# Optimization experiments

Measured on AMD Instinct MI355X. Metric: run time of the kernel, lower is better.

The kernel has to match this reference:

```python
import jax, jax.numpy as jnp
import numpy as np

# Hyperparameters (from init_kwargs)
N = 100000      # num_nodes
T = 4           # num_edge_type
E = 400000      # edges per type
C = 2           # num_channels
L = 2           # num_layers
W_IN = 128      # input feature dim
D = 64          # node_dim (w_out)
NUM_CLASS = 16
BETA = 0.5
M = 10000       # number of target nodes


def setup_inputs() -> dict:
    key = jax.random.key(0)
    ks = jax.random.split(key, 10)
    glorot = np.sqrt(6.0 / (W_IN + D))
    glorot1 = np.sqrt(6.0 / (C * D + D))
    glorot2 = np.sqrt(6.0 / (D + NUM_CLASS))
    return {
        "X": jax.random.normal(ks[0], (N, W_IN), dtype=jnp.float32),
        "edge_value": jax.random.uniform(ks[1], (T, E), dtype=jnp.float32),
        "conv_weights": 0.1 * jax.random.normal(ks[2], (L, C, T), dtype=jnp.float32),
        "Ws": jax.random.uniform(ks[3], (C, W_IN, D), minval=-glorot, maxval=glorot, dtype=jnp.float32),
        "lin1_w": jax.random.uniform(ks[4], (C * D, D), minval=-glorot1, maxval=glorot1, dtype=jnp.float32),
        "lin1_b": jnp.zeros((D,), dtype=jnp.float32),
        "lin_w": jax.random.uniform(ks[5], (D, NUM_CLASS), minval=-glorot2, maxval=glorot2, dtype=jnp.float32),
        "lin_b": jnp.zeros((NUM_CLASS,), dtype=jnp.float32),
        "edge_index": jax.random.randint(ks[6], (T, 2, E), 0, N),
        "target_x": jax.random.randint(ks[7], (M,), 0, N),
    }


def reference(X, edge_value, conv_weights, Ws, lin1_w, lin1_b, lin_w, lin_b,
              edge_index, target_x):
    # Flatten edge types into one big edge list. torch_sparse.coalesce(op='add')
    # followed by torch.sparse.mm is mathematically a duplicate-summing SpMM,
    # i.e. a segment_sum over destination rows.
    rows = edge_index[:, 0, :].reshape(-1)      # [T*E]
    cols = edge_index[:, 1, :].reshape(-1)      # [T*E]
    vals = edge_value.reshape(-1)               # [T*E]
    type_id = jnp.repeat(jnp.arange(T), E)      # [T*E] edge-type id (constant)

    # Per-channel input projections: X_ = X @ Ws[c]  -> [C, N, D]
    X_ = jnp.einsum('nf,cfd->cnd', X, Ws)
    H = X_

    for l in range(L):
        # FastGTConv: softmax over edge types per channel
        filt = jax.nn.softmax(conv_weights[l], axis=1)   # [C, T]
        newH = []
        for c in range(C):
            v = vals * filt[c, type_id]                  # [T*E] mixed edge weights
            msgs = v[:, None] * H[c][cols]               # gather + scale: [T*E, D]
            newH.append(jax.ops.segment_sum(msgs, rows, num_segments=N))
        H = jnp.stack(newH)                              # [C, N, D]

    # FastGTN tail: relu(beta*X_ + (1-beta)*H), concat channels, linear1
    Hc = jax.nn.relu(BETA * X_ + (1.0 - BETA) * H)       # [C, N, D]
    Hcat = jnp.transpose(Hc, (1, 0, 2)).reshape(N, C * D)
    H_ = Hcat @ lin1_w + lin1_b                          # [N, D]

    # FastGTNs head: logits at target nodes
    return H_[target_x] @ lin_w + lin_b                  # [M, NUM_CLASS]
```

## Files before the change

kernel.cpp:

```cpp
#include <hip/hip_runtime.h>

#define N_NODES   100000
#define T_TYPES   4
#define E_EDGES   400000
#define E4        100000
#define G_TOT     400000
#define TE_TOT    1600000
#define C_CH      2
#define L_LAYERS  2
#define W_INF     128
#define DD        64
#define NUM_CLASS 16
#define BETA      0.5f
#define M_TGT     10000

#define NBKT      391
#define BROWS     256
#define BPAD      4864
#define CHUNK_G   1024
#define NPART_BLK 391
#define PROJ_BLK  1563

static const size_t PLANE2 = (size_t)N_NODES * DD;

typedef __attribute__((ext_vector_type(8))) short short8x;
typedef __attribute__((ext_vector_type(4))) float f32x4;

__device__ __forceinline__ unsigned bf16rne(float x) {
    unsigned u = __float_as_uint(x);
    return (u + 0x7FFFu + ((u >> 16) & 1u)) >> 16;
}
__device__ __forceinline__ unsigned packbf(float a, float b) {
    return bf16rne(a) | (bf16rne(b) << 16);
}
__device__ __forceinline__ float bflo(unsigned u) { return __uint_as_float(u << 16); }
__device__ __forceinline__ float bfhi(unsigned u) { return __uint_as_float(u & 0xFFFF0000u); }

__device__ __forceinline__ void load_filter(const float* cw, int layer,
                                            float* f0, float* f1) {
    float m0 = -1e30f, m1 = -1e30f;
    #pragma unroll
    for (int t = 0; t < T_TYPES; ++t) {
        f0[t] = cw[layer * C_CH * T_TYPES + t];
        f1[t] = cw[layer * C_CH * T_TYPES + T_TYPES + t];
        m0 = fmaxf(m0, f0[t]); m1 = fmaxf(m1, f1[t]);
    }
    float s0 = 0.f, s1 = 0.f;
    #pragma unroll
    for (int t = 0; t < T_TYPES; ++t) {
        f0[t] = __expf(f0[t] - m0); s0 += f0[t];
        f1[t] = __expf(f1[t] - m1); s1 += f1[t];
    }
    #pragma unroll
    for (int t = 0; t < T_TYPES; ++t) { f0[t] /= s0; f1[t] /= s1; }
}

__global__ void prep_kernel(const float* __restrict__ Ws,
                            unsigned short* __restrict__ Wsb,
                            int* __restrict__ cursor) {
    int b = blockIdx.x;
    int tid = threadIdx.x;
    if (b < 64) {
        int idx = b * 256 + tid;
        int c   = idx >> 13;
        int rem = idx & 8191;
        int d   = rem >> 7;
        int k   = rem & 127;
        Wsb[idx] = (unsigned short)bf16rne(Ws[c * (W_INF * DD) + k * DD + d]);
    } else {
        int idx = (b - 64) * 256 + tid;
        if (idx < NBKT) cursor[idx] = idx * BPAD;
    }
}

#define AROW 136
#define SMEM_BYTES 45664

__global__ __launch_bounds__(256) void build_proj_kernel(
        const int* __restrict__ edge_index,
        const float* __restrict__ edge_value,
        const float* __restrict__ cw,
        int* __restrict__ cursor,
        int2* __restrict__ edata2,
        const float* __restrict__ X,
        const unsigned short* __restrict__ Wsb,
        unsigned* __restrict__ Xp16) {
    __shared__ __align__(16) char smem[SMEM_BYTES];
    int tid = threadIdx.x;

    if (blockIdx.x < NPART_BLK) {
        int* cnt   = (int*)smem;
        int* lbase = cnt + 392;
        int* gbase = lbase + 392;
        int2* le   = (int2*)(smem + 4704);
        unsigned short* lbk = (unsigned short*)(smem + 4704 + 32768);

        int p = blockIdx.x;
        for (int j = tid; j < NBKT; j += 256) cnt[j] = 0;
        __syncthreads();

        float f0[T_TYPES], f1[T_TYPES];
        load_filter(cw, 0, f0, f1);

        int px[16], pv[16], rk[16], bk[16];
        int ne = 0;
        #pragma unroll
        for (int g = 0; g < 4; ++g) {
            int idx = p * CHUNK_G + g * 256 + tid;
            if (idx < G_TOT) {
                int t = idx / E4, r = idx - t * E4;
                const int* bptr = edge_index + (size_t)t * 2 * E_EDGES;
                int4   rw = ((const int4*)bptr)[r];
                int4   cl = ((const int4*)(bptr + E_EDGES))[r];
                float4 vv = ((const float4*)(edge_value + (size_t)t * E_EDGES))[r];
                int tb = t << 17;
                int   rr[4] = {rw.x, rw.y, rw.z, rw.w};
                int   cc[4] = {cl.x, cl.y, cl.z, cl.w};
                float vf[4] = {vv.x, vv.y, vv.z, vv.w};
                #pragma unroll
                for (int k = 0; k < 4; ++k) {
                    int b = rr[k] >> 8;
                    px[ne] = cc[k] | tb | ((rr[k] & 255) << 19);
                    pv[ne] = __float_as_int(vf[k]);
                    bk[ne] = b;
                    rk[ne] = atomicAdd(&cnt[b], 1);
                    ++ne;
                }
            }
        }
        __syncthreads();
        if (tid < 64) {
            int c[7]; int s = 0;
            #pragma unroll
            for (int k = 0; k < 7; ++k) {
                int idx = tid * 7 + k;
                c[k] = (idx < NBKT) ? cnt[idx] : 0;
                s += c[k];
            }
            int inc = s;
            #pragma unroll
            for (int off = 1; off < 64; off <<= 1) {
                int v = __shfl_up(inc, off);
                if (tid >= off) inc += v;
            }
            int base = inc - s;
            #pragma unroll
            for (int k = 0; k < 7; ++k) {
                int idx = tid * 7 + k;
                if (idx < NBKT) lbase[idx] = base;
                base += c[k];
            }
        }
        __syncthreads();
        #pragma unroll
        for (int k = 0; k < 16; ++k) {
            if (k < ne) {
                int slot = lbase[bk[k]] + rk[k];
                le[slot]  = make_int2(px[k], pv[k]);
                lbk[slot] = (unsigned short)bk[k];
            }
        }
        __syncthreads();
        for (int j = tid; j < NBKT; j += 256)
            gbase[j] = cnt[j] ? atomicAdd(&cursor[j], cnt[j]) : 0;
        __syncthreads();
        int ngrp = min(CHUNK_G, G_TOT - p * CHUNK_G);
        int nloc = 4 * ngrp;
        for (int j = tid; j < nloc; j += 256) {
            int b = lbk[j];
            int2 e = le[j];
            int t = (e.x >> 17) & 3;
            float v = __int_as_float(e.y);
            edata2[gbase[b] + (j - lbase[b])] =
                make_int2(e.x, (int)packbf(v * f0[t], v * f1[t]));
        }
    } else {
        unsigned short* a_lds = (unsigned short*)smem;
        int row0 = (blockIdx.x - NPART_BLK) * 64;

        const float4* X4 = (const float4*)X;
        #pragma unroll
        for (int i = 0; i < 8; ++i) {
            int gi = tid + 256 * i;
            int r  = gi >> 5;
            int c4 = gi & 31;
            int row = row0 + r;
            float4 v = make_float4(0.f, 0.f, 0.f, 0.f);
            if (row < N_NODES) v = X4[(size_t)row * 32 + c4];
            *(uint2*)&a_lds[r * AROW + c4 * 4] = make_uint2(packbf(v.x, v.y),
                                                            packbf(v.z, v.w));
        }
        __syncthreads();

        int wave = tid >> 6, lane = tid & 63;
        int m = lane & 15, q = lane >> 4;

        short8x A[4];
        #pragma unroll
        for (int ks = 0; ks < 4; ++ks)
            A[ks] = *(const short8x*)&a_lds[(wave * 16 + m) * AROW + ks * 32 + q * 8];

        #pragma unroll
        for (int ct = 0; ct < 4; ++ct) {
            f32x4 acc0 = {0.f, 0.f, 0.f, 0.f};
            f32x4 acc1 = {0.f, 0.f, 0.f, 0.f};
            #pragma unroll
            for (int ks = 0; ks < 4; ++ks) {
                short8x B0 = *(const short8x*)(Wsb + (ct * 16 + m) * 128 + ks * 32 + q * 8);
                short8x B1 = *(const short8x*)(Wsb + 8192 + (ct * 16 + m) * 128 + ks * 32 + q * 8);
                acc0 = __builtin_amdgcn_mfma_f32_16x16x32_bf16(A[ks], B0, acc0, 0, 0, 0);
                acc1 = __builtin_amdgcn_mfma_f32_16x16x32_bf16(A[ks], B1, acc1, 0, 0, 0);
            }
            #pragma unroll
            for (int r = 0; r < 4; ++r) {
                int row = row0 + wave * 16 + q * 4 + r;
                if (row < N_NODES)
                    Xp16[(size_t)row * DD + ct * 16 + m] = packbf(acc0[r], acc1[r]);
            }
        }
    }
}

__global__ __launch_bounds__(512) void rowsort_kernel(const int* __restrict__ cursor,
                                                      int2* __restrict__ edata2,
                                                      int* __restrict__ offs) {
    __shared__ int rcnt[BROWS];
    __shared__ int rbase[BROWS];
    __shared__ int rcur[BROWS];
    __shared__ int2 le[BPAD];
    int b   = blockIdx.x;
    int tid = threadIdx.x;
    int bb  = b * BPAD;
    int cnt = cursor[b] - bb;
    if (tid < BROWS) rcnt[tid] = 0;
    __syncthreads();
    for (int j = tid; j < cnt; j += 512) {
        int2 e = edata2[bb + j];
        le[j] = e;
        atomicAdd(&rcnt[(e.x >> 19) & 255], 1);
    }
    __syncthreads();
    if (tid < 64) {
        int c[4]; int s = 0;
        #pragma unroll
        for (int k = 0; k < 4; ++k) { c[k] = rcnt[tid * 4 + k]; s += c[k]; }
        int inc = s;
        #pragma unroll
        for (int off = 1; off < 64; off <<= 1) {
            int v = __shfl_up(inc, off);
            if (tid >= off) inc += v;
        }
        int base = inc - s;
        #pragma unroll
        for (int k = 0; k < 4; ++k) { rbase[tid * 4 + k] = base; base += c[k]; }
    }
    __syncthreads();
    if (tid < BROWS) rcur[tid] = rbase[tid];
    __syncthreads();
    for (int j = tid; j < cnt; j += 512) {
        int2 e = le[j];
        int lr = (e.x >> 19) & 255;
        int pos = atomicAdd(&rcur[lr], 1);
        edata2[bb + pos] = e;
    }
    int row0  = b * BROWS;
    int nrows = min(BROWS, N_NODES - row0);
    if (tid < nrows)
        offs[row0 + tid] = bb + rbase[tid] + rcnt[tid];
}

__device__ __forceinline__ void qfma(const uint4 h, unsigned wp,
                                     float4& a, float4& b) {
    float w0 = bflo(wp), w1 = bfhi(wp);
    a.x = fmaf(w0, bflo(h.x), a.x);
    a.y = fmaf(w1, bfhi(h.x), a.y);
    a.z = fmaf(w0, bflo(h.y), a.z);
    a.w = fmaf(w1, bfhi(h.y), a.w);
    b.x = fmaf(w0, bflo(h.z), b.x);
    b.y = fmaf(w1, bfhi(h.z), b.y);
    b.z = fmaf(w0, bflo(h.w), b.z);
    b.w = fmaf(w1, bfhi(h.w), b.w);
}

__device__ __forceinline__ void qreduce(float4& a, float4& b) {
    a.x += __shfl_xor(a.x, 16); a.y += __shfl_xor(a.y, 16);
    a.z += __shfl_xor(a.z, 16); a.w += __shfl_xor(a.w, 16);
    b.x += __shfl_xor(b.x, 16); b.y += __shfl_xor(b.y, 16);
    b.z += __shfl_xor(b.z, 16); b.w += __shfl_xor(b.w, 16);
    a.x += __shfl_xor(a.x, 32); a.y += __shfl_xor(a.y, 32);
    a.z += __shfl_xor(a.z, 32); a.w += __shfl_xor(a.w, 32);
    b.x += __shfl_xor(b.x, 32); b.y += __shfl_xor(b.y, 32);
    b.z += __shfl_xor(b.z, 32); b.w += __shfl_xor(b.w, 32);
}

__device__ __forceinline__ int row_beg(const int* offs, int row) {
    return ((row & 255) == 0) ? (row >> 8) * BPAD : offs[row - 1];
}

__global__ __launch_bounds__(256) void spmm_gather(const unsigned* __restrict__ Hin16,
                                                   unsigned* __restrict__ Hout16,
                                                   const int* __restrict__ offs,
                                                   const int2* __restrict__ edata2) {
    int lane = threadIdx.x & 63;
    int s16 = lane & 15, sub = lane >> 4;
    int row  = (blockIdx.x * blockDim.x + threadIdx.x) >> 6;
    int beg = row_beg(offs, row);
    int end = offs[row];
    const uint4* hp = (const uint4*)Hin16;
    float4 a = make_float4(0.f, 0.f, 0.f, 0.f);
    float4 b = make_float4(0.f, 0.f, 0.f, 0.f);
    int i = beg + sub;
    for (; i + 4 < end; i += 8) {
        int2 e0 = edata2[i];
        int2 e1 = edata2[i + 4];
        uint4 h0 = hp[(size_t)(e0.x & 0x1FFFF) * 16 + s16];
        uint4 h1 = hp[(size_t)(e1.x & 0x1FFFF) * 16 + s16];
        qfma(h0, (unsigned)e0.y, a, b);
        qfma(h1, (unsigned)e1.y, a, b);
    }
    if (i < end) {
        int2 e = edata2[i];
        uint4 h = hp[(size_t)(e.x & 0x1FFFF) * 16 + s16];
        qfma(h, (unsigned)e.y, a, b);
    }
    qreduce(a, b);
    if (sub == 0)
        ((uint4*)Hout16)[(size_t)row * 16 + s16] =
            make_uint4(packbf(a.x, a.y), packbf(a.z, a.w),
                       packbf(b.x, b.y), packbf(b.z, b.w));
}

__global__ __launch_bounds__(256) void tgt_tail_kernel(const unsigned* __restrict__ Hin16,
                                                       const unsigned* __restrict__ Xp16,
                                                       const int* __restrict__ offs,
                                                       const int2* __restrict__ edata2,
                                                       const float* __restrict__ cw,
                                                       const int* __restrict__ tgt,
                                                       const float* __restrict__ lin1_w,
                                                       const float* __restrict__ lin1_b,
                                                       const float* __restrict__ lin_w,
                                                       const float* __restrict__ lin_b,
                                                       float* __restrict__ out) {
    __shared__ float l1w[W_INF * DD];
    __shared__ float lw[DD * NUM_CLASS];
    __shared__ float l1b[DD];
    __shared__ float lb[NUM_CLASS];
    __shared__ float hc[4][W_INF];
    __shared__ float hmid[4][DD];

    int tid = threadIdx.x;
    {
        const float4* g = (const float4*)lin1_w;
        float4* s = (float4*)l1w;
        #pragma unroll
        for (int i = 0; i < 8; ++i) s[tid + 256 * i] = g[tid + 256 * i];
        ((float4*)lw)[tid] = ((const float4*)lin_w)[tid];
        if (tid < DD) l1b[tid] = lin1_b[tid];
        else if (tid < DD + NUM_CLASS) lb[tid - DD] = lin_b[tid - DD];
    }

    float f0a[T_TYPES], f1a[T_TYPES], f0b[T_TYPES], f1b[T_TYPES];
    load_filter(cw, 0, f0a, f1a);
    load_filter(cw, 1, f0b, f1b);
    float r0[T_TYPES], r1[T_TYPES];
    #pragma unroll
    for (int t = 0; t < T_TYPES; ++t) { r0[t] = f0b[t] / f0a[t]; r1[t] = f1b[t] / f1a[t]; }

    int w = tid >> 6, lane = tid & 63;
    int s16 = lane & 15, sub = lane >> 4;
    int m = blockIdx.x * 4 + w;
    int row = tgt[m];
    int beg = row_beg(offs, row);
    int end = offs[row];
    const uint4* hp = (const uint4*)Hin16;
    float4 a = make_float4(0.f, 0.f, 0.f, 0.f);
    float4 b = make_float4(0.f, 0.f, 0.f, 0.f);
    for (int i = beg + sub; i < end; i += 4) {
        int2 e = edata2[i];
        int t = (e.x >> 17) & 3;
        uint4 h = hp[(size_t)(e.x & 0x1FFFF) * 16 + s16];
        unsigned wp = (unsigned)e.y;
        float w0 = bflo(wp) * r0[t], w1 = bfhi(wp) * r1[t];
        a.x = fmaf(w0, bflo(h.x), a.x);
        a.y = fmaf(w1, bfhi(h.x), a.y);
        a.z = fmaf(w0, bflo(h.y), a.z);
        a.w = fmaf(w1, bfhi(h.y), a.w);
        b.x = fmaf(w0, bflo(h.z), b.x);
        b.y = fmaf(w1, bfhi(h.z), b.y);
        b.z = fmaf(w0, bflo(h.w), b.z);
        b.w = fmaf(w1, bfhi(h.w), b.w);
    }
    qreduce(a, b);

    if (sub == 0) {
        uint4 xu = ((const uint4*)Xp16)[(size_t)row * 16 + s16];
        int d0 = 4 * s16;
        hc[w][d0 + 0]      = fmaxf(BETA * bflo(xu.x) + (1.f - BETA) * a.x, 0.f);
        hc[w][DD + d0 + 0] = fmaxf(BETA * bfhi(xu.x) + (1.f - BETA) * a.y, 0.f);
        hc[w][d0 + 1]      = fmaxf(BETA * bflo(xu.y) + (1.f - BETA) * a.z, 0.f);
        hc[w][DD + d0 + 1] = fmaxf(BETA * bfhi(xu.y) + (1.f - BETA) * a.w, 0.f);
        hc[w][d0 + 2]      = fmaxf(BETA * bflo(xu.z) + (1.f - BETA) * b.x, 0.f);
        hc[w][DD + d0 + 2] = fmaxf(BETA * bfhi(xu.z) + (1.f - BETA) * b.y, 0.f);
        hc[w][d0 + 3]      = fmaxf(BETA * bflo(xu.w) + (1.f - BETA) * b.z, 0.f);
        hc[w][DD + d0 + 3] = fmaxf(BETA * bfhi(xu.w) + (1.f - BETA) * b.w, 0.f);
    }
    __syncthreads();

    float a1 = l1b[lane];
    #pragma unroll 8
    for (int k = 0; k < W_INF; ++k)
        a1 = fmaf(hc[w][k], l1w[k * DD + lane], a1);
    hmid[w][lane] = a1;
    __syncthreads();

    if (lane < NUM_CLASS) {
        float o = lb[lane];
        #pragma unroll 8
        for (int k = 0; k < DD; ++k)
            o = fmaf(hmid[w][k], lw[k * NUM_CLASS + lane], o);
        out[(size_t)m * NUM_CLASS + lane] = o;
    }
}

extern "C" void kernel_launch(void* const* d_in, const int* in_sizes, int n_in,
                              void* d_out, int out_size, void* d_ws, size_t ws_size,
                              hipStream_t stream) {
    const float* X            = (const float*)d_in[0];
    const float* edge_value   = (const float*)d_in[1];
    const float* conv_weights = (const float*)d_in[2];
    const float* Ws           = (const float*)d_in[3];
    const float* lin1_w       = (const float*)d_in[4];
    const float* lin1_b       = (const float*)d_in[5];
    const float* lin_w        = (const float*)d_in[6];
    const float* lin_b        = (const float*)d_in[7];
    const int*   edge_index   = (const int*)d_in[8];
    const int*   target_x     = (const int*)d_in[9];
    float* out = (float*)d_out;

    unsigned*       Xp16 = (unsigned*)d_ws;
    unsigned*       H116 = Xp16 + PLANE2;
    unsigned short* Wsb  = (unsigned short*)(H116 + PLANE2);
    int*            offs = (int*)(Wsb + C_CH * W_INF * DD);
    int*            cursor = offs + N_NODES;
    int2*           edata2 = (int2*)(cursor + 512);

    prep_kernel<<<66, 256, 0, stream>>>(Ws, Wsb, cursor);
    build_proj_kernel<<<NPART_BLK + PROJ_BLK, 256, 0, stream>>>(
        edge_index, edge_value, conv_weights, cursor, edata2, X, Wsb, Xp16);
    rowsort_kernel<<<NBKT, 512, 0, stream>>>(cursor, edata2, offs);
    spmm_gather<<<(N_NODES * 64) / 256, 256, 0, stream>>>(Xp16, H116, offs, edata2);
    tgt_tail_kernel<<<M_TGT / 4, 256, 0, stream>>>(H116, Xp16, offs, edata2,
                                                   conv_weights, target_x,
                                                   lin1_w, lin1_b, lin_w, lin_b, out);
}
```

Measured before the change: 251.9 us.

## Use 64-row buckets and fuse row sort into SpMM gather kernel

```diff
diff --git a/kernel.cpp b/kernel.cpp
--- a/kernel.cpp
+++ b/kernel.cpp
@@ -5,18 +5,16 @@
 #define E_EDGES   400000
 #define E4        100000
 #define G_TOT     400000
-#define TE_TOT    1600000
 #define C_CH      2
-#define L_LAYERS  2
 #define W_INF     128
 #define DD        64
 #define NUM_CLASS 16
 #define BETA      0.5f
 #define M_TGT     10000
 
-#define NBKT      391
-#define BROWS     256
-#define BPAD      4864
+#define NSB       1563
+#define NSB_PAD   1568
+#define SBPAD     1408
 #define CHUNK_G   1024
 #define NPART_BLK 391
 #define PROJ_BLK  1563
@@ -69,12 +67,9 @@
         Wsb[idx] = (unsigned short)bf16rne(Ws[c * (W_INF * DD) + k * DD + d]);
     } else {
         int idx = (b - 64) * 256 + tid;
-        if (idx < NBKT) cursor[idx] = idx * BPAD;
-    }
-}
-
-#define AROW 136
-#define SMEM_BYTES 45664
+        if (idx < NSB) cursor[idx] = idx * SBPAD;
+    }
+}
 
 __global__ __launch_bounds__(256) void build_proj_kernel(
         const int* __restrict__ edge_index,
@@ -85,120 +80,80 @@
         const float* __restrict__ X,
         const unsigned short* __restrict__ Wsb,
         unsigned* __restrict__ Xp16) {
-    __shared__ __align__(16) char smem[SMEM_BYTES];
+    __shared__ int cnt[NSB_PAD];
+    __shared__ int gbase[NSB_PAD];
     int tid = threadIdx.x;
 
     if (blockIdx.x < NPART_BLK) {
-        int* cnt   = (int*)smem;
-        int* lbase = cnt + 392;
-        int* gbase = lbase + 392;
-        int2* le   = (int2*)(smem + 4704);
-        unsigned short* lbk = (unsigned short*)(smem + 4704 + 32768);
-
         int p = blockIdx.x;
-        for (int j = tid; j < NBKT; j += 256) cnt[j] = 0;
+        for (int j = tid; j < NSB; j += 256) cnt[j] = 0;
         __syncthreads();
 
         float f0[T_TYPES], f1[T_TYPES];
         load_filter(cw, 0, f0, f1);
 
-        int px[16], pv[16], rk[16], bk[16];
-        int ne = 0;
+        int px[16], rk[16], bk[16];
+        bool gv[4];
         #pragma unroll
         for (int g = 0; g < 4; ++g) {
             int idx = p * CHUNK_G + g * 256 + tid;
-            if (idx < G_TOT) {
+            gv[g] = idx < G_TOT;
+            if (gv[g]) {
                 int t = idx / E4, r = idx - t * E4;
                 const int* bptr = edge_index + (size_t)t * 2 * E_EDGES;
-                int4   rw = ((const int4*)bptr)[r];
-                int4   cl = ((const int4*)(bptr + E_EDGES))[r];
+                int4 rw = ((const int4*)bptr)[r];
+                int4 cl = ((const int4*)(bptr + E_EDGES))[r];
+                int tb = t << 17;
+                int rr[4] = {rw.x, rw.y, rw.z, rw.w};
+                int cc[4] = {cl.x, cl.y, cl.z, cl.w};
+                #pragma unroll
+                for (int k = 0; k < 4; ++k) {
+                    int kk = g * 4 + k;
+                    int b = rr[k] >> 6;
+                    px[kk] = cc[k] | tb | ((rr[k] & 63) << 19);
+                    bk[kk] = b;
+                    rk[kk] = atomicAdd(&cnt[b], 1);
+                }
+            }
+        }
+        __syncthreads();
+        for (int j = tid; j < NSB; j += 256)
+            gbase[j] = cnt[j] ? atomicAdd(&cursor[j], cnt[j]) : 0;
+        __syncthreads();
+        #pragma unroll
+        for (int g = 0; g < 4; ++g) {
+            if (gv[g]) {
+                int idx = p * CHUNK_G + g * 256 + tid;
+                int t = idx / E4, r = idx - t * E4;
                 float4 vv = ((const float4*)(edge_value + (size_t)t * E_EDGES))[r];
-                int tb = t << 17;
-                int   rr[4] = {rw.x, rw.y, rw.z, rw.w};
-                int   cc[4] = {cl.x, cl.y, cl.z, cl.w};
                 float vf[4] = {vv.x, vv.y, vv.z, vv.w};
                 #pragma unroll
                 for (int k = 0; k < 4; ++k) {
-                    int b = rr[k] >> 8;
-                    px[ne] = cc[k] | tb | ((rr[k] & 255) << 19);
-                    pv[ne] = __float_as_int(vf[k]);
-                    bk[ne] = b;
-                    rk[ne] = atomicAdd(&cnt[b], 1);
-                    ++ne;
+                    int kk = g * 4 + k;
+                    int tt = (px[kk] >> 17) & 3;
+                    edata2[(size_t)gbase[bk[kk]] + rk[kk]] =
+                        make_int2(px[kk], (int)packbf(vf[k] * f0[tt], vf[k] * f1[tt]));
                 }
             }
         }
-        __syncthreads();
-        if (tid < 64) {
-            int c[7]; int s = 0;
-            #pragma unroll
-            for (int k = 0; k < 7; ++k) {
-                int idx = tid * 7 + k;
-                c[k] = (idx < NBKT) ? cnt[idx] : 0;
-                s += c[k];
-            }
-            int inc = s;
-            #pragma unroll
-            for (int off = 1; off < 64; off <<= 1) {
-                int v = __shfl_up(inc, off);
-                if (tid >= off) inc += v;
-            }
-            int base = inc - s;
-            #pragma unroll
-            for (int k = 0; k < 7; ++k) {
-                int idx = tid * 7 + k;
-                if (idx < NBKT) lbase[idx] = base;
-                base += c[k];
-            }
-        }
-        __syncthreads();
-        #pragma unroll
-        for (int k = 0; k < 16; ++k) {
-            if (k < ne) {
-                int slot = lbase[bk[k]] + rk[k];
-                le[slot]  = make_int2(px[k], pv[k]);
-                lbk[slot] = (unsigned short)bk[k];
-            }
-        }
-        __syncthreads();
-        for (int j = tid; j < NBKT; j += 256)
-            gbase[j] = cnt[j] ? atomicAdd(&cursor[j], cnt[j]) : 0;
-        __syncthreads();
-        int ngrp = min(CHUNK_G, G_TOT - p * CHUNK_G);
-        int nloc = 4 * ngrp;
-        for (int j = tid; j < nloc; j += 256) {
-            int b = lbk[j];
-            int2 e = le[j];
-            int t = (e.x >> 17) & 3;
-            float v = __int_as_float(e.y);
-            edata2[gbase[b] + (j - lbase[b])] =
-                make_int2(e.x, (int)packbf(v * f0[t], v * f1[t]));
-        }
     } else {
-        unsigned short* a_lds = (unsigned short*)smem;
         int row0 = (blockIdx.x - NPART_BLK) * 64;
-
-        const float4* X4 = (const float4*)X;
-        #pragma unroll
-        for (int i = 0; i < 8; ++i) {
-            int gi = tid + 256 * i;
-            int r  = gi >> 5;
-            int c4 = gi & 31;
-            int row = row0 + r;
-            float4 v = make_float4(0.f, 0.f, 0.f, 0.f);
-            if (row < N_NODES) v = X4[(size_t)row * 32 + c4];
-            *(uint2*)&a_lds[r * AROW + c4 * 4] = make_uint2(packbf(v.x, v.y),
-                                                            packbf(v.z, v.w));
-        }
-        __syncthreads();
-
         int wave = tid >> 6, lane = tid & 63;
         int m = lane & 15, q = lane >> 4;
-
-        short8x A[4];
-        #pragma unroll
-        for (int ks = 0; ks < 4; ++ks)
-            A[ks] = *(const short8x*)&a_lds[(wave * 16 + m) * AROW + ks * 32 + q * 8];
+        int arow = row0 + wave * 16 + m;
+        const float4* X4 = (const float4*)X;
+        union { short8x s; uint4 u; } A[4];
+        bool valid = arow < N_NODES;
+        #pragma unroll
+        for (int ks = 0; ks < 4; ++ks) {
+            float4 va = make_float4(0.f, 0.f, 0.f, 0.f), vb = va;
+            if (valid) {
+                va = X4[(size_t)arow * 32 + ks * 8 + q * 2];
+                vb = X4[(size_t)arow * 32 + ks * 8 + q * 2 + 1];
+            }
+            A[ks].u = make_uint4(packbf(va.x, va.y), packbf(va.z, va.w),
+                                 packbf(vb.x, vb.y), packbf(vb.z, vb.w));
+        }
 
         #pragma unroll
         for (int ct = 0; ct < 4; ++ct) {
@@ -208,8 +163,8 @@
             for (int ks = 0; ks < 4; ++ks) {
                 short8x B0 = *(const short8x*)(Wsb + (ct * 16 + m) * 128 + ks * 32 + q * 8);
                 short8x B1 = *(const short8x*)(Wsb + 8192 + (ct * 16 + m) * 128 + ks * 32 + q * 8);
-                acc0 = __builtin_amdgcn_mfma_f32_16x16x32_bf16(A[ks], B0, acc0, 0, 0, 0);
-                acc1 = __builtin_amdgcn_mfma_f32_16x16x32_bf16(A[ks], B1, acc1, 0, 0, 0);
+                acc0 = __builtin_amdgcn_mfma_f32_16x16x32_bf16(A[ks].s, B0, acc0, 0, 0, 0);
+                acc1 = __builtin_amdgcn_mfma_f32_16x16x32_bf16(A[ks].s, B1, acc1, 0, 0, 0);
             }
             #pragma unroll
             for (int r = 0; r < 4; ++r) {
@@ -219,54 +174,6 @@
             }
         }
     }
-}
-
-__global__ __launch_bounds__(512) void rowsort_kernel(const int* __restrict__ cursor,
-                                                      int2* __restrict__ edata2,
-                                                      int* __restrict__ offs) {
-    __shared__ int rcnt[BROWS];
-    __shared__ int rbase[BROWS];
-    __shared__ int rcur[BROWS];
-    __shared__ int2 le[BPAD];
-    int b   = blockIdx.x;
-    int tid = threadIdx.x;
-    int bb  = b * BPAD;
-    int cnt = cursor[b] - bb;
-    if (tid < BROWS) rcnt[tid] = 0;
-    __syncthreads();
-    for (int j = tid; j < cnt; j += 512) {
-        int2 e = edata2[bb + j];
-        le[j] = e;
-        atomicAdd(&rcnt[(e.x >> 19) & 255], 1);
-    }
-    __syncthreads();
-    if (tid < 64) {
-        int c[4]; int s = 0;
-        #pragma unroll
-        for (int k = 0; k < 4; ++k) { c[k] = rcnt[tid * 4 + k]; s += c[k]; }
-        int inc = s;
-        #pragma unroll
-        for (int off = 1; off < 64; off <<= 1) {
-            int v = __shfl_up(inc, off);
-            if (tid >= off) inc += v;
-        }
-        int base = inc - s;
-        #pragma unroll
-        for (int k = 0; k < 4; ++k) { rbase[tid * 4 + k] = base; base += c[k]; }
-    }
-    __syncthreads();
-    if (tid < BROWS) rcur[tid] = rbase[tid];
-    __syncthreads();
-    for (int j = tid; j < cnt; j += 512) {
-        int2 e = le[j];
-        int lr = (e.x >> 19) & 255;
-        int pos = atomicAdd(&rcur[lr], 1);
-        edata2[bb + pos] = e;
-    }
-    int row0  = b * BROWS;
-    int nrows = min(BROWS, N_NODES - row0);
-    if (tid < nrows)
-        offs[row0 + tid] = bb + rbase[tid] + rcnt[tid];
 }
 
 __device__ __forceinline__ void qfma(const uint4 h, unsigned wp,
@@ -294,40 +201,86 @@
 }
 
 __device__ __forceinline__ int row_beg(const int* offs, int row) {
-    return ((row & 255) == 0) ? (row >> 8) * BPAD : offs[row - 1];
-}
-
-__global__ __launch_bounds__(256) void spmm_gather(const unsigned* __restrict__ Hin16,
-                                                   unsigned* __restrict__ Hout16,
-                                                   const int* __restrict__ offs,
-                                                   const int2* __restrict__ edata2) {
-    int lane = threadIdx.x & 63;
+    return ((row & 63) == 0) ? (row >> 6) * SBPAD : offs[row - 1];
+}
+
+__global__ __launch_bounds__(256) void sortgather_kernel(
+        const int* __restrict__ cursor,
+        int2* __restrict__ edata2,
+        int* __restrict__ offs,
+        const unsigned* __restrict__ Hin16,
+        unsigned* __restrict__ Hout16) {
+    __shared__ int rcnt[64];
+    __shared__ int rbase[64];
+    __shared__ int rcur[64];
+    __shared__ int2 ls[SBPAD];
+    int tid = threadIdx.x;
+    int sb = blockIdx.x;
+    int base = sb * SBPAD;
+    int cntb = cursor[sb] - base;
+
+    if (tid < 64) rcnt[tid] = 0;
+    __syncthreads();
+    for (int j = tid; j < cntb; j += 256)
+        atomicAdd(&rcnt[(edata2[base + j].x >> 19) & 63], 1);
+    __syncthreads();
+    if (tid < 64) {
+        int c = rcnt[tid];
+        int inc = c;
+        #pragma unroll
+        for (int off = 1; off < 64; off <<= 1) {
+            int v = __shfl_up(inc, off);
+            if (tid >= off) inc += v;
+        }
+        rbase[tid] = inc - c;
+        rcur[tid]  = inc - c;
+    }
+    __syncthreads();
+    for (int j = tid; j < cntb; j += 256) {
+        int2 e = edata2[base + j];
+        int pos = atomicAdd(&rcur[(e.x >> 19) & 63], 1);
+        ls[pos] = e;
+    }
+    __syncthreads();
+
+    for (int j = tid; j < cntb; j += 256) edata2[base + j] = ls[j];
+    int row0 = sb << 6;
+    if (tid < 64) {
+        int row = row0 + tid;
+        if (row < N_NODES) offs[row] = base + rbase[tid] + rcnt[tid];
+    }
+
+    int wv = tid >> 6, lane = tid & 63;
     int s16 = lane & 15, sub = lane >> 4;
-    int row  = (blockIdx.x * blockDim.x + threadIdx.x) >> 6;
-    int beg = row_beg(offs, row);
-    int end = offs[row];
     const uint4* hp = (const uint4*)Hin16;
-    float4 a = make_float4(0.f, 0.f, 0.f, 0.f);
-    float4 b = make_float4(0.f, 0.f, 0.f, 0.f);
-    int i = beg + sub;
-    for (; i + 4 < end; i += 8) {
-        int2 e0 = edata2[i];
-        int2 e1 = edata2[i + 4];
-        uint4 h0 = hp[(size_t)(e0.x & 0x1FFFF) * 16 + s16];
-        uint4 h1 = hp[(size_t)(e1.x & 0x1FFFF) * 16 + s16];
-        qfma(h0, (unsigned)e0.y, a, b);
-        qfma(h1, (unsigned)e1.y, a, b);
-    }
-    if (i < end) {
-        int2 e = edata2[i];
-        uint4 h = hp[(size_t)(e.x & 0x1FFFF) * 16 + s16];
-        qfma(h, (unsigned)e.y, a, b);
-    }
-    qreduce(a, b);
-    if (sub == 0)
-        ((uint4*)Hout16)[(size_t)row * 16 + s16] =
-            make_uint4(packbf(a.x, a.y), packbf(a.z, a.w),
-                       packbf(b.x, b.y), packbf(b.z, b.w));
+    #pragma unroll 1
+    for (int t16 = 0; t16 < 16; ++t16) {
+        int lr = wv * 16 + t16;
+        int beg = rbase[lr];
+        int end = beg + rcnt[lr];
+        float4 a = make_float4(0.f, 0.f, 0.f, 0.f);
+        float4 b = make_float4(0.f, 0.f, 0.f, 0.f);
+        int i = beg + sub;
+        for (; i + 4 < end; i += 8) {
+            int2 e0 = ls[i];
+            int2 e1 = ls[i + 4];
+            uint4 h0 = hp[(size_t)(e0.x & 0x1FFFF) * 16 + s16];
+            uint4 h1 = hp[(size_t)(e1.x & 0x1FFFF) * 16 + s16];
+            qfma(h0, (unsigned)e0.y, a, b);
+            qfma(h1, (unsigned)e1.y, a, b);
+        }
+        if (i < end) {
+            int2 e = ls[i];
+            uint4 h = hp[(size_t)(e.x & 0x1FFFF) * 16 + s16];
+            qfma(h, (unsigned)e.y, a, b);
+        }
+        qreduce(a, b);
+        int row = row0 + lr;
+        if (sub == 0 && row < N_NODES)
+            ((uint4*)Hout16)[(size_t)row * 16 + s16] =
+                make_uint4(packbf(a.x, a.y), packbf(a.z, a.w),
+                           packbf(b.x, b.y), packbf(b.z, b.w));
+    }
 }
 
 __global__ __launch_bounds__(256) void tgt_tail_kernel(const unsigned* __restrict__ Hin16,
@@ -442,13 +395,12 @@
     unsigned short* Wsb  = (unsigned short*)(H116 + PLANE2);
     int*            offs = (int*)(Wsb + C_CH * W_INF * DD);
     int*            cursor = offs + N_NODES;
-    int2*           edata2 = (int2*)(cursor + 512);
-
-    prep_kernel<<<66, 256, 0, stream>>>(Ws, Wsb, cursor);
+    int2*           edata2 = (int2*)(cursor + 1600);
+
+    prep_kernel<<<71, 256, 0, stream>>>(Ws, Wsb, cursor);
     build_proj_kernel<<<NPART_BLK + PROJ_BLK, 256, 0, stream>>>(
         edge_index, edge_value, conv_weights, cursor, edata2, X, Wsb, Xp16);
-    rowsort_kernel<<<NBKT, 512, 0, stream>>>(cursor, edata2, offs);
-    spmm_gather<<<(N_NODES * 64) / 256, 256, 0, stream>>>(Xp16, H116, offs, edata2);
+    sortgather_kernel<<<NSB, 256, 0, stream>>>(cursor, edata2, offs, Xp16, H116);
     tgt_tail_kernel<<<M_TGT / 4, 256, 0, stream>>>(H116, Xp16, offs, edata2,
                                                    conv_weights, target_x,
                                                    lin1_w, lin1_b, lin_w, lin_b, out);
```

Result: no change. 251.9 us (+0.0%).

## Fuse row sort into layer-1 SpMM gather, shrink partition chunks, drop projection LDS staging

Applied to the files above, without the earlier changes.

```diff
diff --git a/kernel.cpp b/kernel.cpp
--- a/kernel.cpp
+++ b/kernel.cpp
@@ -5,9 +5,7 @@
 #define E_EDGES   400000
 #define E4        100000
 #define G_TOT     400000
-#define TE_TOT    1600000
 #define C_CH      2
-#define L_LAYERS  2
 #define W_INF     128
 #define DD        64
 #define NUM_CLASS 16
@@ -17,8 +15,8 @@
 #define NBKT      391
 #define BROWS     256
 #define BPAD      4864
-#define CHUNK_G   1024
-#define NPART_BLK 391
+#define CHUNK_G   512
+#define NPART_BLK 782
 #define PROJ_BLK  1563
 
 static const size_t PLANE2 = (size_t)N_NODES * DD;
@@ -73,9 +71,6 @@
     }
 }
 
-#define AROW 136
-#define SMEM_BYTES 45664
-
 __global__ __launch_bounds__(256) void build_proj_kernel(
         const int* __restrict__ edge_index,
         const float* __restrict__ edge_value,
@@ -85,16 +80,14 @@
         const float* __restrict__ X,
         const unsigned short* __restrict__ Wsb,
         unsigned* __restrict__ Xp16) {
-    __shared__ __align__(16) char smem[SMEM_BYTES];
+    __shared__ int cnt[392];
+    __shared__ int lbase[392];
+    __shared__ int gbase[392];
+    __shared__ int2 le[2048];
+    __shared__ unsigned short lbk[2048];
     int tid = threadIdx.x;
 
     if (blockIdx.x < NPART_BLK) {
-        int* cnt   = (int*)smem;
-        int* lbase = cnt + 392;
-        int* gbase = lbase + 392;
-        int2* le   = (int2*)(smem + 4704);
-        unsigned short* lbk = (unsigned short*)(smem + 4704 + 32768);
-
         int p = blockIdx.x;
         for (int j = tid; j < NBKT; j += 256) cnt[j] = 0;
         __syncthreads();
@@ -102,10 +95,10 @@
         float f0[T_TYPES], f1[T_TYPES];
         load_filter(cw, 0, f0, f1);
 
-        int px[16], pv[16], rk[16], bk[16];
+        int px[8], pv[8], rk[8], bk[8];
         int ne = 0;
         #pragma unroll
-        for (int g = 0; g < 4; ++g) {
+        for (int g = 0; g < 2; ++g) {
             int idx = p * CHUNK_G + g * 256 + tid;
             if (idx < G_TOT) {
                 int t = idx / E4, r = idx - t * E4;
@@ -153,7 +146,7 @@
         }
         __syncthreads();
         #pragma unroll
-        for (int k = 0; k < 16; ++k) {
+        for (int k = 0; k < 8; ++k) {
             if (k < ne) {
                 int slot = lbase[bk[k]] + rk[k];
                 le[slot]  = make_int2(px[k], pv[k]);
@@ -175,30 +168,23 @@
                 make_int2(e.x, (int)packbf(v * f0[t], v * f1[t]));
         }
     } else {
-        unsigned short* a_lds = (unsigned short*)smem;
         int row0 = (blockIdx.x - NPART_BLK) * 64;
-
-        const float4* X4 = (const float4*)X;
-        #pragma unroll
-        for (int i = 0; i < 8; ++i) {
-            int gi = tid + 256 * i;
-            int r  = gi >> 5;
-            int c4 = gi & 31;
-            int row = row0 + r;
-            float4 v = make_float4(0.f, 0.f, 0.f, 0.f);
-            if (row < N_NODES) v = X4[(size_t)row * 32 + c4];
-            *(uint2*)&a_lds[r * AROW + c4 * 4] = make_uint2(packbf(v.x, v.y),
-                                                            packbf(v.z, v.w));
-        }
-        __syncthreads();
-
         int wave = tid >> 6, lane = tid & 63;
         int m = lane & 15, q = lane >> 4;
-
-        short8x A[4];
-        #pragma unroll
-        for (int ks = 0; ks < 4; ++ks)
-            A[ks] = *(const short8x*)&a_lds[(wave * 16 + m) * AROW + ks * 32 + q * 8];
+        int arow = row0 + wave * 16 + m;
+        const float4* X4 = (const float4*)X;
+        union { short8x s; uint4 u; } A[4];
+        bool valid = arow < N_NODES;
+        #pragma unroll
+        for (int ks = 0; ks < 4; ++ks) {
+            float4 va = make_float4(0.f, 0.f, 0.f, 0.f), vb = va;
+            if (valid) {
+                va = X4[(size_t)arow * 32 + ks * 8 + q * 2];
+                vb = X4[(size_t)arow * 32 + ks * 8 + q * 2 + 1];
+            }
+            A[ks].u = make_uint4(packbf(va.x, va.y), packbf(va.z, va.w),
+                                 packbf(vb.x, vb.y), packbf(vb.z, vb.w));
+        }
 
         #pragma unroll
         for (int ct = 0; ct < 4; ++ct) {
@@ -208,8 +194,8 @@
             for (int ks = 0; ks < 4; ++ks) {
                 short8x B0 = *(const short8x*)(Wsb + (ct * 16 + m) * 128 + ks * 32 + q * 8);
                 short8x B1 = *(const short8x*)(Wsb + 8192 + (ct * 16 + m) * 128 + ks * 32 + q * 8);
-                acc0 = __builtin_amdgcn_mfma_f32_16x16x32_bf16(A[ks], B0, acc0, 0, 0, 0);
-                acc1 = __builtin_amdgcn_mfma_f32_16x16x32_bf16(A[ks], B1, acc1, 0, 0, 0);
+                acc0 = __builtin_amdgcn_mfma_f32_16x16x32_bf16(A[ks].s, B0, acc0, 0, 0, 0);
+                acc1 = __builtin_amdgcn_mfma_f32_16x16x32_bf16(A[ks].s, B1, acc1, 0, 0, 0);
             }
             #pragma unroll
             for (int r = 0; r < 4; ++r) {
@@ -219,54 +205,6 @@
             }
         }
     }
-}
-
-__global__ __launch_bounds__(512) void rowsort_kernel(const int* __restrict__ cursor,
-                                                      int2* __restrict__ edata2,
-                                                      int* __restrict__ offs) {
-    __shared__ int rcnt[BROWS];
-    __shared__ int rbase[BROWS];
-    __shared__ int rcur[BROWS];
-    __shared__ int2 le[BPAD];
-    int b   = blockIdx.x;
-    int tid = threadIdx.x;
-    int bb  = b * BPAD;
-    int cnt = cursor[b] - bb;
-    if (tid < BROWS) rcnt[tid] = 0;
-    __syncthreads();
-    for (int j = tid; j < cnt; j += 512) {
-        int2 e = edata2[bb + j];
-        le[j] = e;
-        atomicAdd(&rcnt[(e.x >> 19) & 255], 1);
-    }
-    __syncthreads();
-    if (tid < 64) {
-        int c[4]; int s = 0;
-        #pragma unroll
-        for (int k = 0; k < 4; ++k) { c[k] = rcnt[tid * 4 + k]; s += c[k]; }
-        int inc = s;
-        #pragma unroll
-        for (int off = 1; off < 64; off <<= 1) {
-            int v = __shfl_up(inc, off);
-            if (tid >= off) inc += v;
-        }
-        int base = inc - s;
-        #pragma unroll
-        for (int k = 0; k < 4; ++k) { rbase[tid * 4 + k] = base; base += c[k]; }
-    }
-    __syncthreads();
-    if (tid < BROWS) rcur[tid] = rbase[tid];
-    __syncthreads();
-    for (int j = tid; j < cnt; j += 512) {
-        int2 e = le[j];
-        int lr = (e.x >> 19) & 255;
-        int pos = atomicAdd(&rcur[lr], 1);
-        edata2[bb + pos] = e;
-    }
-    int row0  = b * BROWS;
-    int nrows = min(BROWS, N_NODES - row0);
-    if (tid < nrows)
-        offs[row0 + tid] = bb + rbase[tid] + rcnt[tid];
 }
 
 __device__ __forceinline__ void qfma(const uint4 h, unsigned wp,
@@ -297,40 +235,95 @@
     return ((row & 255) == 0) ? (row >> 8) * BPAD : offs[row - 1];
 }
 
-__global__ __launch_bounds__(256) void spmm_gather(const unsigned* __restrict__ Hin16,
-                                                   unsigned* __restrict__ Hout16,
-                                                   const int* __restrict__ offs,
-                                                   const int2* __restrict__ edata2) {
-    int lane = threadIdx.x & 63;
+__global__ __launch_bounds__(512) void sortgather_kernel(
+        const int* __restrict__ cursor,
+        int2* __restrict__ edata2,
+        int* __restrict__ offs,
+        const unsigned* __restrict__ Hin16,
+        unsigned* __restrict__ Hout16) {
+    __shared__ int rcnt[BROWS];
+    __shared__ int rbase[BROWS];
+    __shared__ int rcur[BROWS];
+    __shared__ int2 ls[BPAD];
+    __shared__ unsigned short sidx[BPAD];
+    int b   = blockIdx.x;
+    int tid = threadIdx.x;
+    int bb  = b * BPAD;
+    int cnt = cursor[b] - bb;
+
+    if (tid < BROWS) rcnt[tid] = 0;
+    __syncthreads();
+    for (int j = tid; j < cnt; j += 512) {
+        int2 e = edata2[bb + j];
+        ls[j] = e;
+        atomicAdd(&rcnt[(e.x >> 19) & 255], 1);
+    }
+    __syncthreads();
+    if (tid < 64) {
+        int c[4]; int s = 0;
+        #pragma unroll
+        for (int k = 0; k < 4; ++k) { c[k] = rcnt[tid * 4 + k]; s += c[k]; }
+        int inc = s;
+        #pragma unroll
+        for (int off = 1; off < 64; off <<= 1) {
+            int v = __shfl_up(inc, off);
+            if (tid >= off) inc += v;
+        }
+        int base = inc - s;
+        #pragma unroll
+        for (int k = 0; k < 4; ++k) { rbase[tid * 4 + k] = base; base += c[k]; }
+    }
+    __syncthreads();
+    if (tid < BROWS) rcur[tid] = rbase[tid];
+    __syncthreads();
+    for (int j = tid; j < cnt; j += 512) {
+        int2 e = ls[j];
+        int lr = (e.x >> 19) & 255;
+        int pos = atomicAdd(&rcur[lr], 1);
+        edata2[bb + pos] = e;
+        sidx[pos] = (unsigned short)j;
+    }
+    int row0 = b * BROWS;
+    if (tid < BROWS && row0 + tid < N_NODES)
+        offs[row0 + tid] = bb + rbase[tid] + rcnt[tid];
+    __syncthreads();
+
+    int wv = tid >> 6, lane = tid & 63;
     int s16 = lane & 15, sub = lane >> 4;
-    int row  = (blockIdx.x * blockDim.x + threadIdx.x) >> 6;
-    int beg = row_beg(offs, row);
-    int end = offs[row];
     const uint4* hp = (const uint4*)Hin16;
-    float4 a = make_float4(0.f, 0.f, 0.f, 0.f);
-    float4 b = make_float4(0.f, 0.f, 0.f, 0.f);
-    int i = beg + sub;
-    for (; i + 4 < end; i += 8) {
-        int2 e0 = edata2[i];
-        int2 e1 = edata2[i + 4];
-        uint4 h0 = hp[(size_t)(e0.x & 0x1FFFF) * 16 + s16];
-        uint4 h1 = hp[(size_t)(e1.x & 0x1FFFF) * 16 + s16];
-        qfma(h0, (unsigned)e0.y, a, b);
-        qfma(h1, (unsigned)e1.y, a, b);
-    }
-    if (i < end) {
-        int2 e = edata2[i];
-        uint4 h = hp[(size_t)(e.x & 0x1FFFF) * 16 + s16];
-        qfma(h, (unsigned)e.y, a, b);
-    }
-    qreduce(a, b);
-    if (sub == 0)
-        ((uint4*)Hout16)[(size_t)row * 16 + s16] =
-            make_uint4(packbf(a.x, a.y), packbf(a.z, a.w),
-                       packbf(b.x, b.y), packbf(b.z, b.w));
-}
-
-__global__ __launch_bounds__(256) void tgt_tail_kernel(const unsigned* __restrict__ Hin16,
+    #pragma unroll 1
+    for (int r32 = 0; r32 < 32; ++r32) {
+        int lr = wv * 32 + r32;
+        int row = row0 + lr;
+        int beg = rbase[lr];
+        int end = beg + rcnt[lr];
+        float4 a = make_float4(0.f, 0.f, 0.f, 0.f);
+        float4 bb4 = make_float4(0.f, 0.f, 0.f, 0.f);
+        int i = beg + sub;
+        for (; i + 4 < end; i += 8) {
+            int j0 = sidx[i];
+            int j1 = sidx[i + 4];
+            int2 e0 = ls[j0];
+            int2 e1 = ls[j1];
+            uint4 h0 = hp[(size_t)(e0.x & 0x1FFFF) * 16 + s16];
+            uint4 h1 = hp[(size_t)(e1.x & 0x1FFFF) * 16 + s16];
+            qfma(h0, (unsigned)e0.y, a, bb4);
+            qfma(h1, (unsigned)e1.y, a, bb4);
+        }
+        if (i < end) {
+            int2 e = ls[sidx[i]];
+            uint4 h = hp[(size_t)(e.x & 0x1FFFF) * 16 + s16];
+            qfma(h, (unsigned)e.y, a, bb4);
+        }
+        qreduce(a, bb4);
+        if (sub == 0 && row < N_NODES)
+            ((uint4*)Hout16)[(size_t)row * 16 + s16] =
+                make_uint4(packbf(a.x, a.y), packbf(a.z, a.w),
+                           packbf(bb4.x, bb4.y), packbf(bb4.z, bb4.w));
+    }
+}
+
+__global__ __launch_bounds__(512) void tgt_tail_kernel(const unsigned* __restrict__ Hin16,
                                                        const unsigned* __restrict__ Xp16,
                                                        const int* __restrict__ offs,
                                                        const int2* __restrict__ edata2,
@@ -345,18 +338,18 @@
     __shared__ float lw[DD * NUM_CLASS];
     __shared__ float l1b[DD];
     __shared__ float lb[NUM_CLASS];
-    __shared__ float hc[4][W_INF];
-    __shared__ float hmid[4][DD];
+    __shared__ float hc[8][W_INF];
+    __shared__ float hmid[8][DD];
 
     int tid = threadIdx.x;
     {
         const float4* g = (const float4*)lin1_w;
         float4* s = (float4*)l1w;
         #pragma unroll
-        for (int i = 0; i < 8; ++i) s[tid + 256 * i] = g[tid + 256 * i];
-        ((float4*)lw)[tid] = ((const float4*)lin_w)[tid];
-        if (tid < DD) l1b[tid] = lin1_b[tid];
-        else if (tid < DD + NUM_CLASS) lb[tid - DD] = lin_b[tid - DD];
+        for (int i = 0; i < 4; ++i) s[tid + 512 * i] = g[tid + 512 * i];
+        if (tid < 256) ((float4*)lw)[tid] = ((const float4*)lin_w)[tid];
+        else if (tid < 256 + DD) l1b[tid - 256] = lin1_b[tid - 256];
+        else if (tid < 256 + DD + NUM_CLASS) lb[tid - 256 - DD] = lin_b[tid - 256 - DD];
     }
 
     float f0a[T_TYPES], f1a[T_TYPES], f0b[T_TYPES], f1b[T_TYPES];
@@ -368,7 +361,7 @@
 
     int w = tid >> 6, lane = tid & 63;
     int s16 = lane & 15, sub = lane >> 4;
-    int m = blockIdx.x * 4 + w;
+    int m = blockIdx.x * 8 + w;
     int row = tgt[m];
     int beg = row_beg(offs, row);
     int end = offs[row];
@@ -447,9 +440,8 @@
     prep_kernel<<<66, 256, 0, stream>>>(Ws, Wsb, cursor);
     build_proj_kernel<<<NPART_BLK + PROJ_BLK, 256, 0, stream>>>(
         edge_index, edge_value, conv_weights, cursor, edata2, X, Wsb, Xp16);
-    rowsort_kernel<<<NBKT, 512, 0, stream>>>(cursor, edata2, offs);
-    spmm_gather<<<(N_NODES * 64) / 256, 256, 0, stream>>>(Xp16, H116, offs, edata2);
-    tgt_tail_kernel<<<M_TGT / 4, 256, 0, stream>>>(H116, Xp16, offs, edata2,
+    sortgather_kernel<<<NBKT, 512, 0, stream>>>(cursor, edata2, offs, Xp16, H116);
+    tgt_tail_kernel<<<M_TGT / 8, 512, 0, stream>>>(H116, Xp16, offs, edata2,
                                                    conv_weights, target_x,
                                                    lin1_w, lin1_b, lin_w, lin_b, out);
 }
```

After: 257.2 us. 1.02x slower.
